# Performance work log

Measured on AMD Instinct MI355X. Metric: run time of the kernel, lower is better.

The kernel has to match this reference:

```python
import jax, jax.numpy as jnp
import numpy as np

B_, C_, H_, W_, N_ = 2, 256, 64, 64, 16


def setup_inputs() -> dict:
    key = jax.random.key(0)
    ks = jax.random.split(key, 6)
    return {
        "features": jax.random.normal(ks[0], (B_, C_, H_, W_), jnp.float32),
        "A_log": jax.random.normal(ks[1], (C_, N_), jnp.float32) * 0.5,
        "D": jax.random.normal(ks[2], (C_,), jnp.float32),
        "W_delta": jax.random.normal(ks[3], (C_, C_), jnp.float32) * 0.02,
        "b_delta": jnp.zeros((C_,), jnp.float32),
        "W_B": jax.random.normal(ks[4], (C_, N_), jnp.float32) * 0.02,
        "W_C": jax.random.normal(ks[5], (C_, N_), jnp.float32) * 0.02,
    }


def _selective_scan(x, A_log, D, W_delta, b_delta, W_B, W_C):
    # x: (B, L, C) -> (B, L, C). Canonical S6 selective scan (mamba corrector).
    delta = jax.nn.softplus(x @ W_delta + b_delta)          # (B, L, C)
    Bm = x @ W_B                                            # (B, L, N)
    Cm = x @ W_C                                            # (B, L, N)
    A = -jnp.exp(A_log)                                     # (C, N), negative real
    dA = jnp.exp(delta[..., None] * A)                      # (B, L, C, N)
    dBx = (delta * x)[..., None] * Bm[:, :, None, :]        # (B, L, C, N)

    def combine(left, right):
        a_l, b_l = left
        a_r, b_r = right
        return (a_l * a_r, a_r * b_l + b_r)

    # h_t = dA_t * h_{t-1} + dBx_t, computed in parallel over L
    _, h = jax.lax.associative_scan(combine, (dA, dBx), axis=1)
    y = jnp.einsum('blcn,bln->blc', h, Cm) + x * D          # (B, L, C)
    return y


def reference(features, A_log, D, W_delta, b_delta, W_B, W_C):
    B, C, H, W = features.shape
    corr = lambda x: _selective_scan(x, A_log, D, W_delta, b_delta, W_B, W_C)

    # direction 1: row-major forward
    flat = features.reshape(B, C, H * W).transpose(0, 2, 1)        # (B, HW, C)
    out1 = corr(flat)
    # direction 2: row-major reversed
    out2 = jnp.flip(corr(jnp.flip(flat, axis=1)), axis=1)
    # direction 3: rows flipped vertically (flip over H), scan, flip back
    rows = features.transpose(0, 2, 3, 1)                          # (B, H, W, C)
    rows_f = jnp.flip(rows, axis=1).reshape(B, H * W, C)
    out3 = jnp.flip(corr(rows_f).reshape(B, H, W, C), axis=1).reshape(B, H * W, C)
    # direction 4: column-major, flipped over W, scan, flip + transpose back
    cols = features.transpose(0, 3, 2, 1)                          # (B, W, H, C)
    cols_f = jnp.flip(cols, axis=1).reshape(B, W * H, C)
    out4 = jnp.flip(corr(cols_f).reshape(B, W, H, C), axis=1)
    out4 = out4.transpose(0, 2, 1, 3).reshape(B, H * W, C)

    mamba_out = (out1 + out2 + out3 + out4) / 4                    # (B, HW, C)
    return mamba_out.transpose(0, 2, 1).reshape(B, C, H, W)
```

## Files before the change

kernel.cpp:

```cpp
#include <hip/hip_runtime.h>
#include <cstdint>
#include <cstddef>

#define BB 2
#define CC 256
#define NN 16
#define LL 4096
#define NCH 128
#define CLEN 32
#define LCH 8
#define LOG2E 1.4426950408889634f

__device__ __forceinline__ float softplus_f(float z) {
    return fmaxf(z, 0.f) + log1pf(expf(-fabsf(z)));
}

__device__ __forceinline__ uint32_t pack_bf2(float d, float u) {
    uint32_t lo = (__float_as_uint(d) + 0x8000u) >> 16;
    uint32_t hh = (__float_as_uint(u) + 0x8000u) & 0xffff0000u;
    return hh | lo;
}

__global__ __launch_bounds__(256) void k1_delta_gemm(
    const float* __restrict__ feat, const float* __restrict__ Wd,
    const float* __restrict__ bd, const float* __restrict__ WB,
    const float* __restrict__ WC, uint32_t* __restrict__ du,
    float* __restrict__ Bm, float* __restrict__ Cm)
{
    int lc = blockIdx.x & 511;
    int b  = blockIdx.x >> 9;
    int l0 = lc * LCH;
    const float* fbase = feat + (size_t)b * CC * LL;

    int c4   = threadIdx.x & 63;
    int kq   = __builtin_amdgcn_readfirstlane(threadIdx.x >> 6);
    int hi   = (threadIdx.x >> 5) & 1;
    int slot = threadIdx.x & 31;
    int mat  = slot >> 4;
    int n    = slot & 15;
    const float* wBC = mat ? WC : WB;

    float accM[8][4] = {};
    float accB[4] = {};

    int kbase = kq * 64;
    #pragma unroll 4
    for (int kk = 0; kk < 64; ++kk) {
        int k = kbase + kk;
        const float* frow = fbase + (size_t)k * LL + l0;
        float4 x0 = *(const float4*)(frow);
        float4 x1 = *(const float4*)(frow + 4);
        float4 wv = *(const float4*)&Wd[(size_t)k * CC + (c4 << 2)];
        float wb  = wBC[k * NN + n];
        float xs[8] = {x0.x, x0.y, x0.z, x0.w, x1.x, x1.y, x1.z, x1.w};
        #pragma unroll
        for (int l = 0; l < 8; ++l) {
            accM[l][0] = fmaf(xs[l], wv.x, accM[l][0]);
            accM[l][1] = fmaf(xs[l], wv.y, accM[l][1]);
            accM[l][2] = fmaf(xs[l], wv.z, accM[l][2]);
            accM[l][3] = fmaf(xs[l], wv.w, accM[l][3]);
        }
        accB[0] = fmaf(hi ? x0.y : x0.x, wb, accB[0]);
        accB[1] = fmaf(hi ? x0.w : x0.z, wb, accB[1]);
        accB[2] = fmaf(hi ? x1.y : x1.x, wb, accB[2]);
        accB[3] = fmaf(hi ? x1.w : x1.z, wb, accB[3]);
    }

    __shared__ float red[4 * 8 * 64 * 4];
    __shared__ float redBC[4 * 2 * 32 * 4];
    #pragma unroll
    for (int l = 0; l < 8; ++l)
        *(float4*)&red[((kq * 8 + l) * 64 + c4) * 4] =
            make_float4(accM[l][0], accM[l][1], accM[l][2], accM[l][3]);
    *(float4*)&redBC[((kq * 2 + hi) * 32 + slot) * 4] =
        make_float4(accB[0], accB[1], accB[2], accB[3]);
    __syncthreads();

    {
        int lr = threadIdx.x >> 5, slotr = threadIdx.x & 31;
        int jj = lr >> 1, hh = lr & 1;
        float s = 0.f;
        #pragma unroll
        for (int q = 0; q < 4; ++q)
            s += redBC[((q * 2 + hh) * 32 + slotr) * 4 + jj];
        int mr = slotr >> 4, nr = slotr & 15;
        (mr ? Cm : Bm)[((size_t)b * LL + l0 + lr) * NN + nr] = s;
    }

    float4 bd4 = *(const float4*)&bd[c4 << 2];
    float2 vx[4];
    #pragma unroll
    for (int j = 0; j < 4; ++j)
        vx[j] = *(const float2*)&fbase[(size_t)(c4 * 4 + j) * LL + l0 + kq * 2];
    #pragma unroll
    for (int lo = 0; lo < 2; ++lo) {
        int l = kq * 2 + lo;
        float z0 = 0.f, z1 = 0.f, z2 = 0.f, z3 = 0.f;
        #pragma unroll
        for (int q = 0; q < 4; ++q) {
            float4 p = *(float4*)&red[((q * 8 + l) * 64 + c4) * 4];
            z0 += p.x; z1 += p.y; z2 += p.z; z3 += p.w;
        }
        float d0 = softplus_f(z0 + bd4.x);
        float d1 = softplus_f(z1 + bd4.y);
        float d2 = softplus_f(z2 + bd4.z);
        float d3 = softplus_f(z3 + bd4.w);
        float x0v = lo ? vx[0].y : vx[0].x;
        float x1v = lo ? vx[1].y : vx[1].x;
        float x2v = lo ? vx[2].y : vx[2].x;
        float x3v = lo ? vx[3].y : vx[3].x;
        uint4 o;
        o.x = pack_bf2(d0, d0 * x0v);
        o.y = pack_bf2(d1, d1 * x1v);
        o.z = pack_bf2(d2, d2 * x2v);
        o.w = pack_bf2(d3, d3 * x3v);
        *(uint4*)&du[((size_t)b * LL + l0 + l) * CC + (c4 << 2)] = o;
    }
}

__global__ __launch_bounds__(256) void p1_aggr(
    const uint32_t* __restrict__ du, const float* __restrict__ Bm,
    const float* __restrict__ A_log, float* __restrict__ P, float* __restrict__ S)
{
    int blk = blockIdx.x;
    int cls = blk >> 8;
    int b   = (blk >> 7) & 1;
    int ch  = blk & 127;
    int p0, inner;
    if (cls == 0)      { p0 = 32 * ch;        inner = 1; }
    else if (cls == 1) { p0 = 4095 - 32 * ch; inner = -1; }
    else               { p0 = 63 - (ch >> 1) + 2048 * (ch & 1); inner = 64; }
    int c = threadIdx.x;
    __shared__ float sBm[CLEN * NN];
    for (int i = threadIdx.x; i < CLEN * NN; i += 256) {
        int j = i >> 4, nn = i & 15;
        sBm[i] = Bm[((size_t)b * LL + (p0 + inner * j)) * NN + nn];
    }
    float A2[NN];
    {
        const float4* al = (const float4*)(A_log + c * NN);
        #pragma unroll
        for (int q = 0; q < 4; ++q) {
            float4 v = al[q];
            A2[q*4+0] = -expf(v.x) * LOG2E;
            A2[q*4+1] = -expf(v.y) * LOG2E;
            A2[q*4+2] = -expf(v.z) * LOG2E;
            A2[q*4+3] = -expf(v.w) * LOG2E;
        }
    }
    __syncthreads();
    const uint32_t* dub = du + (size_t)b * LL * CC + c;
    uint32_t buf[2][8];
    #pragma unroll
    for (int i = 0; i < 8; ++i)
        buf[0][i] = dub[(size_t)(p0 + inner * i) * CC];
    float Sv[NN] = {};
    float sumd = 0.f;
    #pragma unroll
    for (int g = 0; g < 4; ++g) {
        if (g < 3) {
            #pragma unroll
            for (int i = 0; i < 8; ++i)
                buf[(g + 1) & 1][i] = dub[(size_t)(p0 + inner * ((g + 1) * 8 + i)) * CC];
        }
        #pragma unroll
        for (int i = 0; i < 8; ++i) {
            int j = g * 8 + i;
            uint32_t w = buf[g & 1][i];
            float dx = __uint_as_float(w << 16);
            float uy = __uint_as_float(w & 0xffff0000u);
            sumd += dx;
            float dA[NN];
            #pragma unroll
            for (int nn = 0; nn < NN; ++nn) dA[nn] = __builtin_amdgcn_exp2f(A2[nn] * dx);
            #pragma unroll
            for (int nn = 0; nn < NN; ++nn)
                Sv[nn] = fmaf(dA[nn], Sv[nn], uy * sBm[j * 16 + nn]);
        }
    }
    size_t base = ((size_t)((cls * 2 + b) * 128 + ch)) * 4096 + (size_t)c * 16;
    #pragma unroll
    for (int nn = 0; nn < NN; ++nn) {
        P[base + nn] = __builtin_amdgcn_exp2f(A2[nn] * sumd);
        S[base + nn] = Sv[nn];
    }
}

__global__ __launch_bounds__(128) void p2_scan(
    const float* __restrict__ P, const float* __restrict__ S, float* __restrict__ Hin)
{
    int r = blockIdx.x * 128 + threadIdx.x;
    int cn = r & 4095;
    int db = r >> 12;
    int d = db >> 1;
    int cls = (d == 1) ? 1 : ((d == 3) ? 2 : 0);
    int b = db & 1;
    const size_t cbase = ((size_t)(cls * 2 + b) * 128) * 4096 + cn;
    const size_t obase = ((size_t)db * 128) * 4096 + cn;
    float h = 0.f;
    for (int g = 0; g < 16; ++g) {
        float pv[8], sv[8];
        #pragma unroll
        for (int i = 0; i < 8; ++i) {
            int ch = g * 8 + i;
            int chm = (d == 2) ? (126 - 2 * (ch >> 1) + (ch & 1)) : ch;
            size_t ix = cbase + (size_t)chm * 4096;
            pv[i] = P[ix];
            sv[i] = S[ix];
        }
        #pragma unroll
        for (int i = 0; i < 8; ++i) {
            Hin[obase + (size_t)(g * 8 + i) * 4096] = h;
            h = fmaf(pv[i], h, sv[i]);
        }
    }
}

__global__ __launch_bounds__(256) void p3_replay(
    const uint32_t* __restrict__ du, const float* __restrict__ Bm,
    const float* __restrict__ Cm, const float* __restrict__ A_log,
    const float* __restrict__ Hin, float* __restrict__ yA,
    float* __restrict__ yB, float* __restrict__ yC)
{
    int blk = blockIdx.x;
    int sec = blk >> 8;
    int b   = (blk >> 7) & 1;
    int ch  = blk & 127;
    int p0, inner;
    if (sec == 0)      { p0 = 32 * ch;        inner = 1; }
    else if (sec == 1) { p0 = 4095 - 32 * ch; inner = -1; }
    else               { p0 = 63 - (ch >> 1) + 2048 * (ch & 1); inner = 64; }
    int c = threadIdx.x;
    __shared__ float sBm[CLEN * NN];
    __shared__ float sCm[CLEN * NN];
    for (int i = threadIdx.x; i < CLEN * NN; i += 256) {
        int j = i >> 4, nn = i & 15;
        size_t o = ((size_t)b * LL + (p0 + inner * j)) * NN + nn;
        sBm[i] = Bm[o];
        sCm[i] = Cm[o];
    }
    float A2[NN];
    {
        const float4* al = (const float4*)(A_log + c * NN);
        #pragma unroll
        for (int q = 0; q < 4; ++q) {
            float4 v = al[q];
            A2[q*4+0] = -expf(v.x) * LOG2E;
            A2[q*4+1] = -expf(v.y) * LOG2E;
            A2[q*4+2] = -expf(v.z) * LOG2E;
            A2[q*4+3] = -expf(v.w) * LOG2E;
        }
    }
    const uint32_t* dub = du + (size_t)b * LL * CC + c;

    if (sec == 0) {
        int ch2 = 126 - (ch & ~1) + (ch & 1);
        float h0[NN], h2[NN];
        {
            const float4* hp0 = (const float4*)(Hin + ((size_t)(0 * 2 + b) * 128 + ch)  * 4096 + (size_t)c * 16);
            const float4* hp2 = (const float4*)(Hin + ((size_t)(2 * 2 + b) * 128 + ch2) * 4096 + (size_t)c * 16);
            #pragma unroll
            for (int q = 0; q < 4; ++q) {
                float4 v0 = hp0[q], v2 = hp2[q];
                h0[q*4+0]=v0.x; h0[q*4+1]=v0.y; h0[q*4+2]=v0.z; h0[q*4+3]=v0.w;
                h2[q*4+0]=v2.x; h2[q*4+1]=v2.y; h2[q*4+2]=v2.z; h2[q*4+3]=v2.w;
            }
        }
        __syncthreads();
        uint32_t buf[2][8];
        #pragma unroll
        for (int i = 0; i < 8; ++i)
            buf[0][i] = dub[(size_t)(p0 + i) * CC];
        #pragma unroll
        for (int g = 0; g < 4; ++g) {
            if (g < 3) {
                #pragma unroll
                for (int i = 0; i < 8; ++i)
                    buf[(g + 1) & 1][i] = dub[(size_t)(p0 + (g + 1) * 8 + i) * CC];
            }
            #pragma unroll
            for (int i = 0; i < 8; ++i) {
                int j = g * 8 + i;
                uint32_t w = buf[g & 1][i];
                float dx = __uint_as_float(w << 16);
                float uy = __uint_as_float(w & 0xffff0000u);
                float dA[NN];
                #pragma unroll
                for (int nn = 0; nn < NN; ++nn) dA[nn] = __builtin_amdgcn_exp2f(A2[nn] * dx);
                float y0v = 0.f, y2v = 0.f;
                #pragma unroll
                for (int nn = 0; nn < NN; ++nn) {
                    float Bu = uy * sBm[j * 16 + nn];
                    float cm = sCm[j * 16 + nn];
                    h0[nn] = fmaf(dA[nn], h0[nn], Bu);
                    h2[nn] = fmaf(dA[nn], h2[nn], Bu);
                    y0v = fmaf(h0[nn], cm, y0v);
                    y2v = fmaf(h2[nn], cm, y2v);
                }
                yA[((size_t)b * LL + p0 + j) * CC + c] = 0.25f * (y0v + y2v);
            }
        }
    } else {
        int d = (sec == 1) ? 1 : 3;
        float h[NN];
        {
            const float4* hp = (const float4*)(Hin + ((size_t)(d * 2 + b) * 128 + ch) * 4096 + (size_t)c * 16);
            #pragma unroll
            for (int q = 0; q < 4; ++q) {
                float4 v = hp[q];
                h[q*4+0]=v.x; h[q*4+1]=v.y; h[q*4+2]=v.z; h[q*4+3]=v.w;
            }
        }
        __syncthreads();
        float* yD = (sec == 1) ? yB : yC;
        uint32_t buf[2][8];
        #pragma unroll
        for (int i = 0; i < 8; ++i)
            buf[0][i] = dub[(size_t)(p0 + inner * i) * CC];
        #pragma unroll
        for (int g = 0; g < 4; ++g) {
            if (g < 3) {
                #pragma unroll
                for (int i = 0; i < 8; ++i)
                    buf[(g + 1) & 1][i] = dub[(size_t)(p0 + inner * ((g + 1) * 8 + i)) * CC];
            }
            #pragma unroll
            for (int i = 0; i < 8; ++i) {
                int j = g * 8 + i;
                uint32_t w = buf[g & 1][i];
                float dx = __uint_as_float(w << 16);
                float uy = __uint_as_float(w & 0xffff0000u);
                float dA[NN];
                #pragma unroll
                for (int nn = 0; nn < NN; ++nn) dA[nn] = __builtin_amdgcn_exp2f(A2[nn] * dx);
                float yv = 0.f;
                #pragma unroll
                for (int nn = 0; nn < NN; ++nn) {
                    float Bu = uy * sBm[j * 16 + nn];
                    h[nn] = fmaf(dA[nn], h[nn], Bu);
                    yv = fmaf(h[nn], sCm[j * 16 + nn], yv);
                }
                yD[((size_t)b * LL + p0 + inner * j) * CC + c] = 0.25f * yv;
            }
        }
    }
}

__global__ __launch_bounds__(256) void k6_reduce(
    const float* __restrict__ feat, const float* __restrict__ D,
    const float* __restrict__ yA, const float* __restrict__ yB,
    const float* __restrict__ yC, float* __restrict__ out)
{
    int pt = blockIdx.x & 63;
    int ct = (blockIdx.x >> 6) & 3;
    int b  = blockIdx.x >> 8;
    int p0 = pt * 64, c0 = ct * 64;
    __shared__ float tile[64 * 65];
    {
        int cl = threadIdx.x & 63;
        int pg = threadIdx.x >> 6;
        #pragma unroll
        for (int pp = 0; pp < 16; ++pp) {
            int pl = pp * 4 + pg;
            size_t ix = ((size_t)b * LL + p0 + pl) * CC + c0 + cl;
            tile[cl * 65 + pl] = yA[ix] + yB[ix] + yC[ix];
        }
    }
    __syncthreads();
    {
        int pl = threadIdx.x & 63;
        int cg = threadIdx.x >> 6;
        #pragma unroll
        for (int cc = 0; cc < 16; ++cc) {
            int cloc = cc * 4 + cg;
            int c = c0 + cloc;
            size_t o = ((size_t)b * CC + c) * LL + p0 + pl;
            out[o] = tile[cloc * 65 + pl] + feat[o] * D[c];
        }
    }
}

extern "C" void kernel_launch(void* const* d_in, const int* in_sizes, int n_in,
                              void* d_out, int out_size, void* d_ws, size_t ws_size,
                              hipStream_t stream)
{
    const float* feat  = (const float*)d_in[0];
    const float* A_log = (const float*)d_in[1];
    const float* D     = (const float*)d_in[2];
    const float* Wd    = (const float*)d_in[3];
    const float* bd    = (const float*)d_in[4];
    const float* WB    = (const float*)d_in[5];
    const float* WC    = (const float*)d_in[6];
    float* out = (float*)d_out;

    float* ws  = (float*)d_ws;
    uint32_t* du = (uint32_t*)ws;
    float* Bm  = ws  + (size_t)2097152;
    float* Cm  = Bm  + (size_t)131072;
    float* P   = Cm  + (size_t)131072;
    float* S   = P   + (size_t)3145728;
    float* Hin = S   + (size_t)3145728;
    float* yA  = Hin + (size_t)4194304;
    float* yB  = yA  + (size_t)2097152;
    float* yC  = yB  + (size_t)2097152;

    k1_delta_gemm<<<1024, 256, 0, stream>>>(feat, Wd, bd, WB, WC, du, Bm, Cm);
    p1_aggr<<<768, 256, 0, stream>>>(du, Bm, A_log, P, S);
    p2_scan<<<256, 128, 0, stream>>>(P, S, Hin);
    p3_replay<<<768, 256, 0, stream>>>(du, Bm, Cm, A_log, Hin, yA, yB, yC);
    k6_reduce<<<512, 256, 0, stream>>>(feat, D, yA, yB, yC, out);
}
```

Before: 161.2 us.

## Split SSM state dimension across thread pairs in chunk scan kernels

p1_aggr and p3_replay now run 512 threads per block, with two threads per channel. Each thread owns 8 of the 16 state elements, and the output partial sums are combined with a lane shuffle. This halves per-thread register state and serial exp/FMA work and doubles wave parallelism. The cost is duplicated du loads and A_log setup per thread pair, an extra shuffle per timestep, and half the lanes idle on stores.

```diff
diff --git a/kernel.cpp b/kernel.cpp
--- a/kernel.cpp
+++ b/kernel.cpp
@@ -118,7 +118,7 @@
     }
 }
 
-__global__ __launch_bounds__(256) void p1_aggr(
+__global__ __launch_bounds__(512) void p1_aggr(
     const uint32_t* __restrict__ du, const float* __restrict__ Bm,
     const float* __restrict__ A_log, float* __restrict__ P, float* __restrict__ S)
 {
@@ -130,23 +130,23 @@
     if (cls == 0)      { p0 = 32 * ch;        inner = 1; }
     else if (cls == 1) { p0 = 4095 - 32 * ch; inner = -1; }
     else               { p0 = 63 - (ch >> 1) + 2048 * (ch & 1); inner = 64; }
-    int c = threadIdx.x;
+    int c  = threadIdx.x >> 1;
+    int nh = threadIdx.x & 1;
+    int n0 = nh * 8;
     __shared__ float sBm[CLEN * NN];
-    for (int i = threadIdx.x; i < CLEN * NN; i += 256) {
+    {
+        int i = threadIdx.x;
         int j = i >> 4, nn = i & 15;
         sBm[i] = Bm[((size_t)b * LL + (p0 + inner * j)) * NN + nn];
     }
-    float A2[NN];
-    {
-        const float4* al = (const float4*)(A_log + c * NN);
-        #pragma unroll
-        for (int q = 0; q < 4; ++q) {
-            float4 v = al[q];
-            A2[q*4+0] = -expf(v.x) * LOG2E;
-            A2[q*4+1] = -expf(v.y) * LOG2E;
-            A2[q*4+2] = -expf(v.z) * LOG2E;
-            A2[q*4+3] = -expf(v.w) * LOG2E;
-        }
+    float A2[8];
+    {
+        const float4* al = (const float4*)(A_log + c * NN + n0);
+        float4 v0 = al[0], v1 = al[1];
+        A2[0] = -expf(v0.x) * LOG2E; A2[1] = -expf(v0.y) * LOG2E;
+        A2[2] = -expf(v0.z) * LOG2E; A2[3] = -expf(v0.w) * LOG2E;
+        A2[4] = -expf(v1.x) * LOG2E; A2[5] = -expf(v1.y) * LOG2E;
+        A2[6] = -expf(v1.z) * LOG2E; A2[7] = -expf(v1.w) * LOG2E;
     }
     __syncthreads();
     const uint32_t* dub = du + (size_t)b * LL * CC + c;
@@ -154,7 +154,7 @@
     #pragma unroll
     for (int i = 0; i < 8; ++i)
         buf[0][i] = dub[(size_t)(p0 + inner * i) * CC];
-    float Sv[NN] = {};
+    float Sv[8] = {};
     float sumd = 0.f;
     #pragma unroll
     for (int g = 0; g < 4; ++g) {
@@ -170,17 +170,17 @@
             float dx = __uint_as_float(w << 16);
             float uy = __uint_as_float(w & 0xffff0000u);
             sumd += dx;
-            float dA[NN];
+            float dA[8];
             #pragma unroll
-            for (int nn = 0; nn < NN; ++nn) dA[nn] = __builtin_amdgcn_exp2f(A2[nn] * dx);
+            for (int nn = 0; nn < 8; ++nn) dA[nn] = __builtin_amdgcn_exp2f(A2[nn] * dx);
             #pragma unroll
-            for (int nn = 0; nn < NN; ++nn)
-                Sv[nn] = fmaf(dA[nn], Sv[nn], uy * sBm[j * 16 + nn]);
-        }
-    }
-    size_t base = ((size_t)((cls * 2 + b) * 128 + ch)) * 4096 + (size_t)c * 16;
-    #pragma unroll
-    for (int nn = 0; nn < NN; ++nn) {
+            for (int nn = 0; nn < 8; ++nn)
+                Sv[nn] = fmaf(dA[nn], Sv[nn], uy * sBm[j * 16 + n0 + nn]);
+        }
+    }
+    size_t base = ((size_t)((cls * 2 + b) * 128 + ch)) * 4096 + (size_t)c * 16 + n0;
+    #pragma unroll
+    for (int nn = 0; nn < 8; ++nn) {
         P[base + nn] = __builtin_amdgcn_exp2f(A2[nn] * sumd);
         S[base + nn] = Sv[nn];
     }
@@ -216,7 +216,7 @@
     }
 }
 
-__global__ __launch_bounds__(256) void p3_replay(
+__global__ __launch_bounds__(512) void p3_replay(
     const uint32_t* __restrict__ du, const float* __restrict__ Bm,
     const float* __restrict__ Cm, const float* __restrict__ A_log,
     const float* __restrict__ Hin, float* __restrict__ yA,
@@ -230,41 +230,40 @@
     if (sec == 0)      { p0 = 32 * ch;        inner = 1; }
     else if (sec == 1) { p0 = 4095 - 32 * ch; inner = -1; }
     else               { p0 = 63 - (ch >> 1) + 2048 * (ch & 1); inner = 64; }
-    int c = threadIdx.x;
+    int c  = threadIdx.x >> 1;
+    int nh = threadIdx.x & 1;
+    int n0 = nh * 8;
     __shared__ float sBm[CLEN * NN];
     __shared__ float sCm[CLEN * NN];
-    for (int i = threadIdx.x; i < CLEN * NN; i += 256) {
+    {
+        int i = threadIdx.x;
         int j = i >> 4, nn = i & 15;
         size_t o = ((size_t)b * LL + (p0 + inner * j)) * NN + nn;
         sBm[i] = Bm[o];
         sCm[i] = Cm[o];
     }
-    float A2[NN];
-    {
-        const float4* al = (const float4*)(A_log + c * NN);
-        #pragma unroll
-        for (int q = 0; q < 4; ++q) {
-            float4 v = al[q];
-            A2[q*4+0] = -expf(v.x) * LOG2E;
-            A2[q*4+1] = -expf(v.y) * LOG2E;
-            A2[q*4+2] = -expf(v.z) * LOG2E;
-            A2[q*4+3] = -expf(v.w) * LOG2E;
-        }
+    float A2[8];
+    {
+        const float4* al = (const float4*)(A_log + c * NN + n0);
+        float4 v0 = al[0], v1 = al[1];
+        A2[0] = -expf(v0.x) * LOG2E; A2[1] = -expf(v0.y) * LOG2E;
+        A2[2] = -expf(v0.z) * LOG2E; A2[3] = -expf(v0.w) * LOG2E;
+        A2[4] = -expf(v1.x) * LOG2E; A2[5] = -expf(v1.y) * LOG2E;
+        A2[6] = -expf(v1.z) * LOG2E; A2[7] = -expf(v1.w) * LOG2E;
     }
     const uint32_t* dub = du + (size_t)b * LL * CC + c;
 
     if (sec == 0) {
         int ch2 = 126 - (ch & ~1) + (ch & 1);
-        float h0[NN], h2[NN];
+        float h0[8], h2[8];
         {
-            const float4* hp0 = (const float4*)(Hin + ((size_t)(0 * 2 + b) * 128 + ch)  * 4096 + (size_t)c * 16);
-            const float4* hp2 = (const float4*)(Hin + ((size_t)(2 * 2 + b) * 128 + ch2) * 4096 + (size_t)c * 16);
-            #pragma unroll
-            for (int q = 0; q < 4; ++q) {
-                float4 v0 = hp0[q], v2 = hp2[q];
-                h0[q*4+0]=v0.x; h0[q*4+1]=v0.y; h0[q*4+2]=v0.z; h0[q*4+3]=v0.w;
-                h2[q*4+0]=v2.x; h2[q*4+1]=v2.y; h2[q*4+2]=v2.z; h2[q*4+3]=v2.w;
-            }
+            const float4* hp0 = (const float4*)(Hin + ((size_t)(0 * 2 + b) * 128 + ch)  * 4096 + (size_t)c * 16 + n0);
+            const float4* hp2 = (const float4*)(Hin + ((size_t)(2 * 2 + b) * 128 + ch2) * 4096 + (size_t)c * 16 + n0);
+            float4 v0 = hp0[0], v1 = hp0[1], w0 = hp2[0], w1 = hp2[1];
+            h0[0]=v0.x; h0[1]=v0.y; h0[2]=v0.z; h0[3]=v0.w;
+            h0[4]=v1.x; h0[5]=v1.y; h0[6]=v1.z; h0[7]=v1.w;
+            h2[0]=w0.x; h2[1]=w0.y; h2[2]=w0.z; h2[3]=w0.w;
+            h2[4]=w1.x; h2[5]=w1.y; h2[6]=w1.z; h2[7]=w1.w;
         }
         __syncthreads();
         uint32_t buf[2][8];
@@ -284,32 +283,31 @@
                 uint32_t w = buf[g & 1][i];
                 float dx = __uint_as_float(w << 16);
                 float uy = __uint_as_float(w & 0xffff0000u);
-                float dA[NN];
-                #pragma unroll
-                for (int nn = 0; nn < NN; ++nn) dA[nn] = __builtin_amdgcn_exp2f(A2[nn] * dx);
-                float y0v = 0.f, y2v = 0.f;
-                #pragma unroll
-                for (int nn = 0; nn < NN; ++nn) {
-                    float Bu = uy * sBm[j * 16 + nn];
-                    float cm = sCm[j * 16 + nn];
+                float dA[8];
+                #pragma unroll
+                for (int nn = 0; nn < 8; ++nn) dA[nn] = __builtin_amdgcn_exp2f(A2[nn] * dx);
+                float part = 0.f;
+                #pragma unroll
+                for (int nn = 0; nn < 8; ++nn) {
+                    float Bu = uy * sBm[j * 16 + n0 + nn];
+                    float cm = sCm[j * 16 + n0 + nn];
                     h0[nn] = fmaf(dA[nn], h0[nn], Bu);
                     h2[nn] = fmaf(dA[nn], h2[nn], Bu);
-                    y0v = fmaf(h0[nn], cm, y0v);
-                    y2v = fmaf(h2[nn], cm, y2v);
+                    part = fmaf(h0[nn] + h2[nn], cm, part);
                 }
-                yA[((size_t)b * LL + p0 + j) * CC + c] = 0.25f * (y0v + y2v);
+                float tot = part + __shfl_xor(part, 1, 64);
+                if (nh == 0)
+                    yA[((size_t)b * LL + p0 + j) * CC + c] = 0.25f * tot;
             }
         }
     } else {
         int d = (sec == 1) ? 1 : 3;
-        float h[NN];
+        float h[8];
         {
-            const float4* hp = (const float4*)(Hin + ((size_t)(d * 2 + b) * 128 + ch) * 4096 + (size_t)c * 16);
-            #pragma unroll
-            for (int q = 0; q < 4; ++q) {
-                float4 v = hp[q];
-                h[q*4+0]=v.x; h[q*4+1]=v.y; h[q*4+2]=v.z; h[q*4+3]=v.w;
-            }
+            const float4* hp = (const float4*)(Hin + ((size_t)(d * 2 + b) * 128 + ch) * 4096 + (size_t)c * 16 + n0);
+            float4 v0 = hp[0], v1 = hp[1];
+            h[0]=v0.x; h[1]=v0.y; h[2]=v0.z; h[3]=v0.w;
+            h[4]=v1.x; h[5]=v1.y; h[6]=v1.z; h[7]=v1.w;
         }
         __syncthreads();
         float* yD = (sec == 1) ? yB : yC;
@@ -330,17 +328,19 @@
                 uint32_t w = buf[g & 1][i];
                 float dx = __uint_as_float(w << 16);
                 float uy = __uint_as_float(w & 0xffff0000u);
-                float dA[NN];
-                #pragma unroll
-                for (int nn = 0; nn < NN; ++nn) dA[nn] = __builtin_amdgcn_exp2f(A2[nn] * dx);
-                float yv = 0.f;
-                #pragma unroll
-                for (int nn = 0; nn < NN; ++nn) {
-                    float Bu = uy * sBm[j * 16 + nn];
+                float dA[8];
+                #pragma unroll
+                for (int nn = 0; nn < 8; ++nn) dA[nn] = __builtin_amdgcn_exp2f(A2[nn] * dx);
+                float part = 0.f;
+                #pragma unroll
+                for (int nn = 0; nn < 8; ++nn) {
+                    float Bu = uy * sBm[j * 16 + n0 + nn];
                     h[nn] = fmaf(dA[nn], h[nn], Bu);
-                    yv = fmaf(h[nn], sCm[j * 16 + nn], yv);
+                    part = fmaf(h[nn], sCm[j * 16 + n0 + nn], part);
                 }
-                yD[((size_t)b * LL + p0 + inner * j) * CC + c] = 0.25f * yv;
+                float tot = part + __shfl_xor(part, 1, 64);
+                if (nh == 0)
+                    yD[((size_t)b * LL + p0 + inner * j) * CC + c] = 0.25f * tot;
             }
         }
     }
@@ -405,8 +405,8 @@
     float* yC  = yB  + (size_t)2097152;
 
     k1_delta_gemm<<<1024, 256, 0, stream>>>(feat, Wd, bd, WB, WC, du, Bm, Cm);
-    p1_aggr<<<768, 256, 0, stream>>>(du, Bm, A_log, P, S);
+    p1_aggr<<<768, 512, 0, stream>>>(du, Bm, A_log, P, S);
     p2_scan<<<256, 128, 0, stream>>>(P, S, Hin);
-    p3_replay<<<768, 256, 0, stream>>>(du, Bm, Cm, A_log, Hin, yA, yB, yC);
+    p3_replay<<<768, 512, 0, stream>>>(du, Bm, Cm, A_log, Hin, yA, yB, yC);
     k6_reduce<<<512, 256, 0, stream>>>(feat, D, yA, yB, yC, out);
 }
```

After: 165.9 us. +2.9%, slower.

## Merge forward and reverse row scans per chunk, halve chunk length

Applied to the files above, without the earlier changes.

The chunked scan now uses 256 chunks of 16 steps instead of 128 of 32. Each row block handles the forward and reversed row directions together, reusing the loaded du values and the Bm/Cm tiles in shared memory and staging the forward outputs in shared memory. This removes one separate pass over du and one output buffer, and the reduce kernel reads two y arrays instead of three. The inter-chunk scan becomes twice as long and the P/S/Hin workspaces grow, which adds memory traffic and serial work in p2.

```diff
diff --git a/kernel.cpp b/kernel.cpp
--- a/kernel.cpp
+++ b/kernel.cpp
@@ -6,8 +6,8 @@
 #define CC 256
 #define NN 16
 #define LL 4096
-#define NCH 128
-#define CLEN 32
+#define NCH 256
+#define CL 16
 #define LCH 8
 #define LOG2E 1.4426950408889634f
 
@@ -120,22 +120,21 @@
 
 __global__ __launch_bounds__(256) void p1_aggr(
     const uint32_t* __restrict__ du, const float* __restrict__ Bm,
-    const float* __restrict__ A_log, float* __restrict__ P, float* __restrict__ S)
+    const float* __restrict__ A_log, float* __restrict__ Prow,
+    float* __restrict__ Sf, float* __restrict__ Sb,
+    float* __restrict__ Pcol, float* __restrict__ Scol)
 {
     int blk = blockIdx.x;
-    int cls = blk >> 8;
-    int b   = (blk >> 7) & 1;
-    int ch  = blk & 127;
-    int p0, inner;
-    if (cls == 0)      { p0 = 32 * ch;        inner = 1; }
-    else if (cls == 1) { p0 = 4095 - 32 * ch; inner = -1; }
-    else               { p0 = 63 - (ch >> 1) + 2048 * (ch & 1); inner = 64; }
     int c = threadIdx.x;
-    __shared__ float sBm[CLEN * NN];
-    for (int i = threadIdx.x; i < CLEN * NN; i += 256) {
-        int j = i >> 4, nn = i & 15;
-        sBm[i] = Bm[((size_t)b * LL + (p0 + inner * j)) * NN + nn];
-    }
+    bool isRow = blk < 512;
+    int b, ch, p0, inner;
+    if (isRow) { b = blk >> 8; ch = blk & 255; p0 = ch * CL; inner = 1; }
+    else { int t = blk - 512; b = t >> 8; ch = t & 255;
+           p0 = 63 - (ch >> 2) + 1024 * (ch & 3); inner = 64; }
+
+    __shared__ float sBm[CL * NN];
+    { int j = c >> 4, nn = c & 15;
+      sBm[c] = Bm[((size_t)b * LL + (p0 + inner * j)) * NN + nn]; }
     float A2[NN];
     {
         const float4* al = (const float4*)(A_log + c * NN);
@@ -150,63 +149,80 @@
     }
     __syncthreads();
     const uint32_t* dub = du + (size_t)b * LL * CC + c;
-    uint32_t buf[2][8];
-    #pragma unroll
-    for (int i = 0; i < 8; ++i)
-        buf[0][i] = dub[(size_t)(p0 + inner * i) * CC];
-    float Sv[NN] = {};
+    uint32_t w[CL];
+    #pragma unroll
+    for (int j = 0; j < CL; ++j)
+        w[j] = dub[(size_t)(p0 + inner * j) * CC];
+
+    float Svf[NN] = {};
     float sumd = 0.f;
     #pragma unroll
-    for (int g = 0; g < 4; ++g) {
-        if (g < 3) {
-            #pragma unroll
-            for (int i = 0; i < 8; ++i)
-                buf[(g + 1) & 1][i] = dub[(size_t)(p0 + inner * ((g + 1) * 8 + i)) * CC];
-        }
-        #pragma unroll
-        for (int i = 0; i < 8; ++i) {
-            int j = g * 8 + i;
-            uint32_t w = buf[g & 1][i];
-            float dx = __uint_as_float(w << 16);
-            float uy = __uint_as_float(w & 0xffff0000u);
-            sumd += dx;
+    for (int j = 0; j < CL; ++j) {
+        float dx = __uint_as_float(w[j] << 16);
+        float uy = __uint_as_float(w[j] & 0xffff0000u);
+        sumd += dx;
+        float dA[NN];
+        #pragma unroll
+        for (int nn = 0; nn < NN; ++nn) dA[nn] = __builtin_amdgcn_exp2f(A2[nn] * dx);
+        #pragma unroll
+        for (int nn = 0; nn < NN; ++nn)
+            Svf[nn] = fmaf(dA[nn], Svf[nn], uy * sBm[j * 16 + nn]);
+    }
+    size_t base = ((size_t)(b * 256 + ch)) * 4096 + (size_t)c * 16;
+    if (isRow) {
+        float Svb[NN] = {};
+        #pragma unroll
+        for (int j = CL - 1; j >= 0; --j) {
+            float dx = __uint_as_float(w[j] << 16);
+            float uy = __uint_as_float(w[j] & 0xffff0000u);
             float dA[NN];
             #pragma unroll
             for (int nn = 0; nn < NN; ++nn) dA[nn] = __builtin_amdgcn_exp2f(A2[nn] * dx);
             #pragma unroll
             for (int nn = 0; nn < NN; ++nn)
-                Sv[nn] = fmaf(dA[nn], Sv[nn], uy * sBm[j * 16 + nn]);
-        }
-    }
-    size_t base = ((size_t)((cls * 2 + b) * 128 + ch)) * 4096 + (size_t)c * 16;
-    #pragma unroll
-    for (int nn = 0; nn < NN; ++nn) {
-        P[base + nn] = __builtin_amdgcn_exp2f(A2[nn] * sumd);
-        S[base + nn] = Sv[nn];
+                Svb[nn] = fmaf(dA[nn], Svb[nn], uy * sBm[j * 16 + nn]);
+        }
+        #pragma unroll
+        for (int nn = 0; nn < NN; ++nn) {
+            Prow[base + nn] = __builtin_amdgcn_exp2f(A2[nn] * sumd);
+            Sf[base + nn]   = Svf[nn];
+            Sb[base + nn]   = Svb[nn];
+        }
+    } else {
+        #pragma unroll
+        for (int nn = 0; nn < NN; ++nn) {
+            Pcol[base + nn] = __builtin_amdgcn_exp2f(A2[nn] * sumd);
+            Scol[base + nn] = Svf[nn];
+        }
     }
 }
 
 __global__ __launch_bounds__(128) void p2_scan(
-    const float* __restrict__ P, const float* __restrict__ S, float* __restrict__ Hin)
+    const float* __restrict__ Prow, const float* __restrict__ Sf,
+    const float* __restrict__ Sb, const float* __restrict__ Pcol,
+    const float* __restrict__ Scol, float* __restrict__ Hin)
 {
     int r = blockIdx.x * 128 + threadIdx.x;
     int cn = r & 4095;
     int db = r >> 12;
     int d = db >> 1;
-    int cls = (d == 1) ? 1 : ((d == 3) ? 2 : 0);
     int b = db & 1;
-    const size_t cbase = ((size_t)(cls * 2 + b) * 128) * 4096 + cn;
-    const size_t obase = ((size_t)db * 128) * 4096 + cn;
+    const float* Pp = (d == 3) ? Pcol : Prow;
+    const float* Sp = (d == 3) ? Scol : ((d == 1) ? Sb : Sf);
+    const size_t obase = ((size_t)db * 256) * 4096 + cn;
     float h = 0.f;
-    for (int g = 0; g < 16; ++g) {
+    for (int g = 0; g < 32; ++g) {
         float pv[8], sv[8];
         #pragma unroll
         for (int i = 0; i < 8; ++i) {
             int ch = g * 8 + i;
-            int chm = (d == 2) ? (126 - 2 * (ch >> 1) + (ch & 1)) : ch;
-            size_t ix = cbase + (size_t)chm * 4096;
-            pv[i] = P[ix];
-            sv[i] = S[ix];
+            int chm;
+            if (d == 1)      chm = 255 - ch;
+            else if (d == 2) chm = (63 - (ch >> 2)) * 4 + (ch & 3);
+            else             chm = ch;
+            size_t ix = ((size_t)(b * 256 + chm)) * 4096 + cn;
+            pv[i] = Pp[ix];
+            sv[i] = Sp[ix];
         }
         #pragma unroll
         for (int i = 0; i < 8; ++i) {
@@ -219,26 +235,24 @@
 __global__ __launch_bounds__(256) void p3_replay(
     const uint32_t* __restrict__ du, const float* __restrict__ Bm,
     const float* __restrict__ Cm, const float* __restrict__ A_log,
-    const float* __restrict__ Hin, float* __restrict__ yA,
-    float* __restrict__ yB, float* __restrict__ yC)
+    const float* __restrict__ Hin, float* __restrict__ yR,
+    float* __restrict__ yC)
 {
     int blk = blockIdx.x;
-    int sec = blk >> 8;
-    int b   = (blk >> 7) & 1;
-    int ch  = blk & 127;
-    int p0, inner;
-    if (sec == 0)      { p0 = 32 * ch;        inner = 1; }
-    else if (sec == 1) { p0 = 4095 - 32 * ch; inner = -1; }
-    else               { p0 = 63 - (ch >> 1) + 2048 * (ch & 1); inner = 64; }
     int c = threadIdx.x;
-    __shared__ float sBm[CLEN * NN];
-    __shared__ float sCm[CLEN * NN];
-    for (int i = threadIdx.x; i < CLEN * NN; i += 256) {
-        int j = i >> 4, nn = i & 15;
-        size_t o = ((size_t)b * LL + (p0 + inner * j)) * NN + nn;
-        sBm[i] = Bm[o];
-        sCm[i] = Cm[o];
-    }
+    bool isRow = blk < 512;
+    int b, ch, p0, inner;
+    if (isRow) { b = blk >> 8; ch = blk & 255; p0 = ch * CL; inner = 1; }
+    else { int t = blk - 512; b = t >> 8; ch = t & 255;
+           p0 = 63 - (ch >> 2) + 1024 * (ch & 3); inner = 64; }
+
+    __shared__ float sBm[CL * NN];
+    __shared__ float sCm[CL * NN];
+    __shared__ float sY[CL * CC];
+    { int j = c >> 4, nn = c & 15;
+      size_t o = ((size_t)b * LL + (p0 + inner * j)) * NN + nn;
+      sBm[c] = Bm[o];
+      sCm[c] = Cm[o]; }
     float A2[NN];
     {
         const float4* al = (const float4*)(A_log + c * NN);
@@ -251,14 +265,19 @@
             A2[q*4+3] = -expf(v.w) * LOG2E;
         }
     }
+    __syncthreads();
     const uint32_t* dub = du + (size_t)b * LL * CC + c;
-
-    if (sec == 0) {
-        int ch2 = 126 - (ch & ~1) + (ch & 1);
+    uint32_t w[CL];
+    #pragma unroll
+    for (int j = 0; j < CL; ++j)
+        w[j] = dub[(size_t)(p0 + inner * j) * CC];
+
+    if (isRow) {
+        int g2 = (63 - (ch >> 2)) * 4 + (ch & 3);
         float h0[NN], h2[NN];
         {
-            const float4* hp0 = (const float4*)(Hin + ((size_t)(0 * 2 + b) * 128 + ch)  * 4096 + (size_t)c * 16);
-            const float4* hp2 = (const float4*)(Hin + ((size_t)(2 * 2 + b) * 128 + ch2) * 4096 + (size_t)c * 16);
+            const float4* hp0 = (const float4*)(Hin + ((size_t)((0 * 2 + b) * 256 + ch) * 4096) + (size_t)c * 16);
+            const float4* hp2 = (const float4*)(Hin + ((size_t)((2 * 2 + b) * 256 + g2) * 4096) + (size_t)c * 16);
             #pragma unroll
             for (int q = 0; q < 4; ++q) {
                 float4 v0 = hp0[q], v2 = hp2[q];
@@ -266,90 +285,82 @@
                 h2[q*4+0]=v2.x; h2[q*4+1]=v2.y; h2[q*4+2]=v2.z; h2[q*4+3]=v2.w;
             }
         }
-        __syncthreads();
-        uint32_t buf[2][8];
-        #pragma unroll
-        for (int i = 0; i < 8; ++i)
-            buf[0][i] = dub[(size_t)(p0 + i) * CC];
-        #pragma unroll
-        for (int g = 0; g < 4; ++g) {
-            if (g < 3) {
-                #pragma unroll
-                for (int i = 0; i < 8; ++i)
-                    buf[(g + 1) & 1][i] = dub[(size_t)(p0 + (g + 1) * 8 + i) * CC];
-            }
-            #pragma unroll
-            for (int i = 0; i < 8; ++i) {
-                int j = g * 8 + i;
-                uint32_t w = buf[g & 1][i];
-                float dx = __uint_as_float(w << 16);
-                float uy = __uint_as_float(w & 0xffff0000u);
-                float dA[NN];
-                #pragma unroll
-                for (int nn = 0; nn < NN; ++nn) dA[nn] = __builtin_amdgcn_exp2f(A2[nn] * dx);
-                float y0v = 0.f, y2v = 0.f;
-                #pragma unroll
-                for (int nn = 0; nn < NN; ++nn) {
-                    float Bu = uy * sBm[j * 16 + nn];
-                    float cm = sCm[j * 16 + nn];
-                    h0[nn] = fmaf(dA[nn], h0[nn], Bu);
-                    h2[nn] = fmaf(dA[nn], h2[nn], Bu);
-                    y0v = fmaf(h0[nn], cm, y0v);
-                    y2v = fmaf(h2[nn], cm, y2v);
-                }
-                yA[((size_t)b * LL + p0 + j) * CC + c] = 0.25f * (y0v + y2v);
-            }
+        #pragma unroll
+        for (int j = 0; j < CL; ++j) {
+            float dx = __uint_as_float(w[j] << 16);
+            float uy = __uint_as_float(w[j] & 0xffff0000u);
+            float dA[NN];
+            #pragma unroll
+            for (int nn = 0; nn < NN; ++nn) dA[nn] = __builtin_amdgcn_exp2f(A2[nn] * dx);
+            float yv = 0.f;
+            #pragma unroll
+            for (int nn = 0; nn < NN; ++nn) {
+                float Bu = uy * sBm[j * 16 + nn];
+                float cm = sCm[j * 16 + nn];
+                h0[nn] = fmaf(dA[nn], h0[nn], Bu);
+                h2[nn] = fmaf(dA[nn], h2[nn], Bu);
+                yv = fmaf(h0[nn] + h2[nn], cm, yv);
+            }
+            sY[j * CC + c] = yv;
+        }
+        float h1[NN];
+        {
+            const float4* hp1 = (const float4*)(Hin + ((size_t)((1 * 2 + b) * 256 + (255 - ch)) * 4096) + (size_t)c * 16);
+            #pragma unroll
+            for (int q = 0; q < 4; ++q) {
+                float4 v = hp1[q];
+                h1[q*4+0]=v.x; h1[q*4+1]=v.y; h1[q*4+2]=v.z; h1[q*4+3]=v.w;
+            }
+        }
+        #pragma unroll
+        for (int j = CL - 1; j >= 0; --j) {
+            float dx = __uint_as_float(w[j] << 16);
+            float uy = __uint_as_float(w[j] & 0xffff0000u);
+            float dA[NN];
+            #pragma unroll
+            for (int nn = 0; nn < NN; ++nn) dA[nn] = __builtin_amdgcn_exp2f(A2[nn] * dx);
+            float y1 = 0.f;
+            #pragma unroll
+            for (int nn = 0; nn < NN; ++nn) {
+                float Bu = uy * sBm[j * 16 + nn];
+                h1[nn] = fmaf(dA[nn], h1[nn], Bu);
+                y1 = fmaf(h1[nn], sCm[j * 16 + nn], y1);
+            }
+            yR[((size_t)b * LL + p0 + j) * CC + c] = 0.25f * (sY[j * CC + c] + y1);
         }
     } else {
-        int d = (sec == 1) ? 1 : 3;
         float h[NN];
         {
-            const float4* hp = (const float4*)(Hin + ((size_t)(d * 2 + b) * 128 + ch) * 4096 + (size_t)c * 16);
+            const float4* hp = (const float4*)(Hin + ((size_t)((3 * 2 + b) * 256 + ch) * 4096) + (size_t)c * 16);
             #pragma unroll
             for (int q = 0; q < 4; ++q) {
                 float4 v = hp[q];
                 h[q*4+0]=v.x; h[q*4+1]=v.y; h[q*4+2]=v.z; h[q*4+3]=v.w;
             }
         }
-        __syncthreads();
-        float* yD = (sec == 1) ? yB : yC;
-        uint32_t buf[2][8];
-        #pragma unroll
-        for (int i = 0; i < 8; ++i)
-            buf[0][i] = dub[(size_t)(p0 + inner * i) * CC];
-        #pragma unroll
-        for (int g = 0; g < 4; ++g) {
-            if (g < 3) {
-                #pragma unroll
-                for (int i = 0; i < 8; ++i)
-                    buf[(g + 1) & 1][i] = dub[(size_t)(p0 + inner * ((g + 1) * 8 + i)) * CC];
-            }
-            #pragma unroll
-            for (int i = 0; i < 8; ++i) {
-                int j = g * 8 + i;
-                uint32_t w = buf[g & 1][i];
-                float dx = __uint_as_float(w << 16);
-                float uy = __uint_as_float(w & 0xffff0000u);
-                float dA[NN];
-                #pragma unroll
-                for (int nn = 0; nn < NN; ++nn) dA[nn] = __builtin_amdgcn_exp2f(A2[nn] * dx);
-                float yv = 0.f;
-                #pragma unroll
-                for (int nn = 0; nn < NN; ++nn) {
-                    float Bu = uy * sBm[j * 16 + nn];
-                    h[nn] = fmaf(dA[nn], h[nn], Bu);
-                    yv = fmaf(h[nn], sCm[j * 16 + nn], yv);
-                }
-                yD[((size_t)b * LL + p0 + inner * j) * CC + c] = 0.25f * yv;
-            }
+        #pragma unroll
+        for (int j = 0; j < CL; ++j) {
+            float dx = __uint_as_float(w[j] << 16);
+            float uy = __uint_as_float(w[j] & 0xffff0000u);
+            float dA[NN];
+            #pragma unroll
+            for (int nn = 0; nn < NN; ++nn) dA[nn] = __builtin_amdgcn_exp2f(A2[nn] * dx);
+            float yv = 0.f;
+            #pragma unroll
+            for (int nn = 0; nn < NN; ++nn) {
+                float Bu = uy * sBm[j * 16 + nn];
+                h[nn] = fmaf(dA[nn], h[nn], Bu);
+                yv = fmaf(h[nn], sCm[j * 16 + nn], yv);
+            }
+            yC[((size_t)b * LL + p0 + inner * j) * CC + c] = 0.25f * yv;
         }
     }
 }
 
 __global__ __launch_bounds__(256) void k6_reduce(
     const float* __restrict__ feat, const float* __restrict__ D,
-    const float* __restrict__ yA, const float* __restrict__ yB,
-    const float* __restrict__ yC, float* __restrict__ out)
+    const float* __restrict__ yR, const float* __restrict__ yC,
+    float* __restrict__ out)
 {
     int pt = blockIdx.x & 63;
     int ct = (blockIdx.x >> 6) & 3;
@@ -363,7 +374,7 @@
         for (int pp = 0; pp < 16; ++pp) {
             int pl = pp * 4 + pg;
             size_t ix = ((size_t)b * LL + p0 + pl) * CC + c0 + cl;
-            tile[cl * 65 + pl] = yA[ix] + yB[ix] + yC[ix];
+            tile[cl * 65 + pl] = yR[ix] + yC[ix];
         }
     }
     __syncthreads();
@@ -395,18 +406,20 @@
 
     float* ws  = (float*)d_ws;
     uint32_t* du = (uint32_t*)ws;
-    float* Bm  = ws  + (size_t)2097152;
-    float* Cm  = Bm  + (size_t)131072;
-    float* P   = Cm  + (size_t)131072;
-    float* S   = P   + (size_t)3145728;
-    float* Hin = S   + (size_t)3145728;
-    float* yA  = Hin + (size_t)4194304;
-    float* yB  = yA  + (size_t)2097152;
-    float* yC  = yB  + (size_t)2097152;
+    float* Bm   = ws   + (size_t)2097152;
+    float* Cm   = Bm   + (size_t)131072;
+    float* Prow = Cm   + (size_t)131072;
+    float* Sf   = Prow + (size_t)2097152;
+    float* Sb   = Sf   + (size_t)2097152;
+    float* Pcol = Sb   + (size_t)2097152;
+    float* Scol = Pcol + (size_t)2097152;
+    float* Hin  = Scol + (size_t)2097152;
+    float* yR   = Hin  + (size_t)8388608;
+    float* yC   = yR   + (size_t)2097152;
 
     k1_delta_gemm<<<1024, 256, 0, stream>>>(feat, Wd, bd, WB, WC, du, Bm, Cm);
-    p1_aggr<<<768, 256, 0, stream>>>(du, Bm, A_log, P, S);
-    p2_scan<<<256, 128, 0, stream>>>(P, S, Hin);
-    p3_replay<<<768, 256, 0, stream>>>(du, Bm, Cm, A_log, Hin, yA, yB, yC);
-    k6_reduce<<<512, 256, 0, stream>>>(feat, D, yA, yB, yC, out);
-}
+    p1_aggr<<<1024, 256, 0, stream>>>(du, Bm, A_log, Prow, Sf, Sb, Pcol, Scol);
+    p2_scan<<<256, 128, 0, stream>>>(Prow, Sf, Sb, Pcol, Scol, Hin);
+    p3_replay<<<1024, 256, 0, stream>>>(du, Bm, Cm, A_log, Hin, yR, yC);
+    k6_reduce<<<512, 256, 0, stream>>>(feat, D, yR, yC, out);
+}
```

New measurement: 241.8 us. 1.5x slower.
